# Kernel tuning notes

Measured on AMD Instinct MI355X. Metric: run time of the kernel, lower is better.

## Reference

```python
import jax, jax.numpy as jnp
import numpy as np

N, E = 100000, 3200000
IN, HID, OUT, ED = 16, 64, 32, 3
BN_EPS = 1e-5


def setup_inputs() -> dict:
    key = jax.random.key(0)
    ks = jax.random.split(key, 40)
    d = {}
    d["x"] = jax.random.normal(ks[0], (N, IN), jnp.float32)
    d["edge_index"] = jax.random.randint(ks[1], (2, E), 0, N, dtype=jnp.int32)
    d["edge_attr"] = jax.random.normal(ks[2], (E, ED), jnp.float32)
    i = [3]
    def p(shape):
        w = jax.random.normal(ks[i[0]], shape, jnp.float32) * 0.05
        i[0] += 1
        return w
    for tag, nd in (("inj1", IN), ("inj2", HID), ("inj3", HID)):
        d[tag + "_w1"] = p((ED, nd)); d[tag + "_b1"] = p((nd,))
        d[tag + "_w2"] = p((nd, nd)); d[tag + "_b2"] = p((nd,))
    for tag, ci, co in (("conv1", IN, HID), ("conv2", HID, HID), ("conv3", HID, OUT)):
        d[tag + "_wl"] = p((ci, co)); d[tag + "_bl"] = p((co,))
        d[tag + "_wr"] = p((ci, co))
    for tag, c in (("bn1", HID), ("bn2", HID), ("bn3", OUT)):
        d[tag + "_w"] = p((c,)); d[tag + "_b"] = p((c,))
    return d


def _inject(x, src, dst, edge_attr, w1, b1, w2, b2):
    # edge MLP: [E, ED] -> [E, node_dim], sigmoid wind gate from column 2
    h = jax.nn.relu(edge_attr @ w1 + b1) @ w2 + b2
    gate = jax.nn.sigmoid(edge_attr[:, 2:3])
    msg = h * gate
    agg = jax.ops.segment_sum(msg, dst, num_segments=x.shape[0])
    return x + agg


def _sage(x, src, dst, wl, bl, wr):
    # PyG SAGEConv (mean aggr): lin_l(mean_{j in N(i)} x_j) + lin_r(x_i)
    n = x.shape[0]
    s = jax.ops.segment_sum(x[src], dst, num_segments=n)
    cnt = jax.ops.segment_sum(jnp.ones((src.shape[0], 1), x.dtype), dst, num_segments=n)
    mean = s / jnp.maximum(cnt, 1.0)
    return mean @ wl + bl + x @ wr


def _bn(x, w, b):
    # eval-mode BatchNorm with running_mean=0, running_var=1
    return x * (w / jnp.sqrt(1.0 + BN_EPS)) + b


def reference(x, edge_index, edge_attr,
              inj1_w1, inj1_b1, inj1_w2, inj1_b2,
              inj2_w1, inj2_b1, inj2_w2, inj2_b2,
              inj3_w1, inj3_b1, inj3_w2, inj3_b2,
              conv1_wl, conv1_bl, conv1_wr,
              conv2_wl, conv2_bl, conv2_wr,
              conv3_wl, conv3_bl, conv3_wr,
              bn1_w, bn1_b, bn2_w, bn2_b, bn3_w, bn3_b):
    src, dst = edge_index[0], edge_index[1]
    h = _inject(x, src, dst, edge_attr, inj1_w1, inj1_b1, inj1_w2, inj1_b2)
    h = jax.nn.relu(_bn(_sage(h, src, dst, conv1_wl, conv1_bl, conv1_wr), bn1_w, bn1_b))
    h = _inject(h, src, dst, edge_attr, inj2_w1, inj2_b1, inj2_w2, inj2_b2)
    h = jax.nn.relu(_bn(_sage(h, src, dst, conv2_wl, conv2_bl, conv2_wr), bn2_w, bn2_b))
    h = _inject(h, src, dst, edge_attr, inj3_w1, inj3_b1, inj3_w2, inj3_b2)
    h = jax.nn.relu(_bn(_sage(h, src, dst, conv3_wl, conv3_bl, conv3_wr), bn3_w, bn3_b))
    return h
```

## Files before the change

kernel.cpp:

```cpp
#include <hip/hip_runtime.h>
#include <math.h>

#define N_NODES 100000
#define N_EDGES 3200000
#define NB 391
#define CHUNK 3072
#define NCHUNK 1042
#define HCHUNK 4096
#define NHCHUNK 782
#define CAPB 10240

constexpr size_t al512(size_t x){ return (x + 511) & ~size_t(511); }
constexpr size_t o_bcnt = 0;
constexpr size_t o_bst  = al512(o_bcnt + 512*4);
constexpr size_t o_gb   = al512(o_bst  + 512*4);
constexpr size_t o_off  = al512(o_gb   + 512*4);
constexpr size_t o_srcp = al512(o_off  + ((size_t)N_NODES+1)*4);
constexpr size_t o_epk  = al512(o_srcp + (size_t)N_EDGES*4);
constexpr size_t o_U1   = al512(o_epk  + (size_t)N_EDGES*16);
constexpr size_t o_U2   = al512(o_U1   + (size_t)N_NODES*16*4);
constexpr size_t o_U3   = o_U2 + (size_t)N_NODES*64*4;
constexpr size_t o_gs   = al512(o_U3   + (size_t)N_NODES*64*4);
constexpr size_t o_h1   = al512(o_gs   + (size_t)N_NODES*4);
constexpr size_t o_m1   = al512(o_h1   + (size_t)N_NODES*16*4);
constexpr size_t o_rec  = o_U2;
constexpr size_t o_h2bf = o_epk;
constexpr size_t o_h3bf = o_epk + (size_t)N_NODES*128;
constexpr size_t o_m2   = o_U2;
constexpr size_t o_m3   = o_U2;

#define BN_RSQRT 0.9999950000374997f

__device__ __forceinline__ float4 ld4(const float* p){ return *(const float4*)p; }
__device__ __forceinline__ float fc(const float4& v, int i){ return ((const float*)&v)[i]; }
__device__ __forceinline__ float uf(unsigned u){ return __uint_as_float(u); }

__device__ __forceinline__ unsigned f2bf(float x){
    unsigned u = __float_as_uint(x);
    u += 0x7fffu + ((u >> 16) & 1u);
    return u >> 16;
}

__global__ __launch_bounds__(256) void khistBin(const int* __restrict__ dst,
                                                int* __restrict__ binCnt){
    __shared__ int c[NB];
    int t = threadIdx.x;
    for(int i=t; i<NB; i+=256) c[i] = 0;
    __syncthreads();
    long base = (long)blockIdx.x*HCHUNK;
    int nrem = (int)(N_EDGES - base); if(nrem > HCHUNK) nrem = HCHUNK;
    for(int k=t; k<nrem; k+=256)
        atomicAdd(&c[dst[base+k] >> 8], 1);
    __syncthreads();
    for(int i=t; i<NB; i+=256)
        if(c[i]) atomicAdd(&binCnt[i], c[i]);
}

__global__ __launch_bounds__(512) void kscanBin(const int* __restrict__ binCnt,
                                                int* __restrict__ binStart,
                                                int* __restrict__ gbase){
    __shared__ int s[512];
    int t = threadIdx.x;
    int v = (t < NB) ? binCnt[t] : 0;
    s[t] = v; __syncthreads();
    for(int off=1; off<512; off<<=1){
        int a = (t>=off) ? s[t-off] : 0;
        __syncthreads(); s[t] += a; __syncthreads();
    }
    int ex = (t==0) ? 0 : s[t-1];
    if(t < NB){ binStart[t] = ex; gbase[t] = ex; }
    if(t == NB) binStart[NB] = s[NB-1];
}

__global__ __launch_bounds__(256) void kbinA(const int* __restrict__ src,
                                             const int* __restrict__ dst,
                                             const float* __restrict__ ea,
                                             int* __restrict__ gbase,
                                             unsigned* __restrict__ recD){
    __shared__ int cnt[NB], lofs[NB], gst[NB], lcnt[NB];
    __shared__ int sscan[256];
    __shared__ unsigned stage[CHUNK*4];
    __shared__ unsigned short binOf[CHUNK];
    int t = threadIdx.x;
    long e0i = (long)blockIdx.x*CHUNK;
    int nrem = (int)(N_EDGES - e0i); if(nrem > CHUNK) nrem = CHUNK;
    if(nrem <= 0) return;

    for(int b=t; b<NB; b+=256){ cnt[b]=0; lcnt[b]=0; }
    __syncthreads();
    for(int k=t; k<nrem; k+=256)
        atomicAdd(&cnt[dst[e0i+k] >> 8], 1);
    __syncthreads();
    int c0 = (2*t   < NB) ? cnt[2*t]   : 0;
    int c1 = (2*t+1 < NB) ? cnt[2*t+1] : 0;
    sscan[t] = c0 + c1;
    __syncthreads();
    for(int off=1; off<256; off<<=1){
        int v = (t>=off) ? sscan[t-off] : 0;
        __syncthreads(); sscan[t] += v; __syncthreads();
    }
    int base = (t==0) ? 0 : sscan[t-1];
    if(2*t   < NB) lofs[2*t]   = base;
    if(2*t+1 < NB) lofs[2*t+1] = base + c0;
    for(int b=t; b<NB; b+=256){
        int c = cnt[b];
        gst[b] = c ? atomicAdd(&gbase[b], c) : 0;
    }
    __syncthreads();
    for(int k=t; k<nrem; k+=256){
        long i = e0i + k;
        int d = dst[i];
        int s = src[i];
        float a0 = ea[i*3+0], a1 = ea[i*3+1], a2 = ea[i*3+2];
        int b = d >> 8;
        int p = lofs[b] + atomicAdd(&lcnt[b], 1);
        stage[4*p+0] = (unsigned)s | ((unsigned)(d & 255) << 17);
        stage[4*p+1] = __float_as_uint(a0);
        stage[4*p+2] = __float_as_uint(a1);
        stage[4*p+3] = __float_as_uint(a2);
        binOf[p] = (unsigned short)b;
    }
    __syncthreads();
    int total4 = nrem*4;
    for(int q=t; q<total4; q+=256){
        int p = q >> 2;
        int b = binOf[p];
        int g = gst[b] + (p - lofs[b]);
        recD[(size_t)4*g + (q & 3)] = stage[q];
    }
}

__global__ __launch_bounds__(512) void kbinB(const uint4* __restrict__ rec4,
                                             const int* __restrict__ binStart,
                                             int* __restrict__ offs,
                                             int* __restrict__ srcp,
                                             float4* __restrict__ epk){
    __shared__ int pfx[257], lcnt[256];
    __shared__ int sscan[256];
    __shared__ unsigned short perm[CAPB];
    __shared__ unsigned char  nibOf[CAPB];
    int t = threadIdx.x;
    int b = blockIdx.x;
    int n0 = b*256;
    int nn = N_NODES - n0; if(nn > 256) nn = 256;
    int base = binStart[b];
    int m    = binStart[b+1] - base;
    for(int i=t; i<256; i+=512) lcnt[i] = 0;
    __syncthreads();
    for(int p=t; p<m; p+=512){
        unsigned w0 = ((const unsigned*)rec4)[(size_t)4*(base+p)];
        int nib = (int)((w0 >> 17) & 255u);
        if(p < CAPB) nibOf[p] = (unsigned char)nib;
        atomicAdd(&lcnt[nib], 1);
    }
    __syncthreads();
    if(t < 256) sscan[t] = lcnt[t];
    __syncthreads();
    if(t < 256){
        for(int off=1; off<256; off<<=1){
            int v = (t>=off) ? sscan[t-off] : 0;
            __syncthreads(); sscan[t] += v; __syncthreads();
        }
        pfx[t+1] = sscan[t];
        if(t==0) pfx[0] = 0;
    } else {
        for(int off=1; off<256; off<<=1){ __syncthreads(); __syncthreads(); }
    }
    __syncthreads();
    for(int i=t; i<=nn; i+=512) offs[n0+i] = base + pfx[i];
    for(int i=t; i<256; i+=512) lcnt[i] = 0;
    __syncthreads();
    for(int p=t; p<m; p+=512){
        int nib = nibOf[p];
        int slot = pfx[nib] + atomicAdd(&lcnt[nib], 1);
        perm[slot] = (unsigned short)p;
    }
    __syncthreads();
    for(int s=t; s<m; s+=512){
        uint4 r = rec4[(size_t)(base + (int)perm[s])];
        float e2 = uf(r.w);
        float gate = __builtin_amdgcn_rcpf(1.f + __expf(-e2));
        srcp[base+s] = (int)(r.x & 0x1FFFFu);
        epk [base+s] = make_float4(uf(r.y), uf(r.z), e2, gate);
    }
}

struct InjW { float wa1,wb1,wc1,bb1, wa2,wb2,wc2,bb2, wa3,wb3,wc3,bb3; };

__device__ __forceinline__ void edge_acc(const float4& r, const InjW& W,
                                         float& a1, float& a2, float& a3, float& g){
    float h1 = fmaf(r.z,W.wc1, fmaf(r.y,W.wb1, fmaf(r.x,W.wa1, W.bb1)));
    float h2 = fmaf(r.z,W.wc2, fmaf(r.y,W.wb2, fmaf(r.x,W.wa2, W.bb2)));
    float h3 = fmaf(r.z,W.wc3, fmaf(r.y,W.wb3, fmaf(r.x,W.wa3, W.bb3)));
    a1 = fmaf(fmaxf(h1,0.f), r.w, a1);
    a2 = fmaf(fmaxf(h2,0.f), r.w, a2);
    a3 = fmaf(fmaxf(h3,0.f), r.w, a3);
    g += r.w;
}

__global__ void kinject(const float4* __restrict__ epk, const int* __restrict__ offs,
                        const float* __restrict__ w11, const float* __restrict__ b11,
                        const float* __restrict__ w12, const float* __restrict__ b12,
                        const float* __restrict__ w13, const float* __restrict__ b13,
                        float* __restrict__ U1, float* __restrict__ U2,
                        float* __restrict__ U3, float* __restrict__ gsum){
    int gid = blockIdx.x*blockDim.x + threadIdx.x;
    int node = gid >> 6;
    if(node >= N_NODES) return;
    int lane = threadIdx.x & 63;
    int l16  = lane & 15;
    InjW W;
    W.wa1=w11[l16];  W.wb1=w11[16+l16];  W.wc1=w11[32+l16];  W.bb1=b11[l16];
    W.wa2=w12[lane]; W.wb2=w12[64+lane]; W.wc2=w12[128+lane]; W.bb2=b12[lane];
    W.wa3=w13[lane]; W.wb3=w13[64+lane]; W.wc3=w13[128+lane]; W.bb3=b13[lane];
    int beg = offs[node], end = offs[node+1];
    float a1=0.f, a2=0.f, a3=0.f, g=0.f;
    int e = beg;
    for(; e+2<=end; e+=2){
        float4 r0 = epk[e];
        float4 r1 = epk[e+1];
        edge_acc(r0, W, a1, a2, a3, g);
        edge_acc(r1, W, a1, a2, a3, g);
    }
    if(e < end) edge_acc(epk[e], W, a1, a2, a3, g);
    U2[(size_t)node*64 + lane] = a2;
    U3[(size_t)node*64 + lane] = a3;
    if(lane < 16) U1[node*16 + l16] = a1;
    if(lane == 0) gsum[node] = g;
}

__global__ void kgather16(const float* __restrict__ h, const int* __restrict__ srcp,
                          const int* __restrict__ offs, float* __restrict__ m){
    int gid = blockIdx.x*blockDim.x + threadIdx.x;
    int node = gid >> 6;
    if(node >= N_NODES) return;
    int lane = threadIdx.x & 63;
    int q = lane >> 4, d = lane & 15;
    int beg = offs[node], end = offs[node+1];
    float acc = 0.f;
    for(int e=beg+q; e<end; e+=4) acc += h[(size_t)srcp[e]*16 + d];
    acc += __shfl_down(acc, 32);
    acc += __shfl_down(acc, 16);
    if(lane < 16){
        float c = fmaxf((float)(end-beg), 1.f);
        m[node*16 + lane] = acc / c;
    }
}

__global__ void kgather64bf(const unsigned* __restrict__ hbf, const int* __restrict__ srcp,
                            const int* __restrict__ offs, float* __restrict__ m){
    int gid = blockIdx.x*blockDim.x + threadIdx.x;
    int node = gid >> 6;
    if(node >= N_NODES) return;
    int lane = threadIdx.x & 63;
    int half = lane >> 5, c = lane & 31;
    int beg = offs[node], end = offs[node+1];
    float acc0 = 0.f, acc1 = 0.f;
    int e = beg;
    for(; e+4<=end; e+=4){
        int s0 = srcp[e+half], s1 = srcp[e+2+half];
        unsigned w0 = hbf[(size_t)s0*32 + c];
        unsigned w1 = hbf[(size_t)s1*32 + c];
        acc0 += uf(w0<<16); acc1 += uf(w0 & 0xffff0000u);
        acc0 += uf(w1<<16); acc1 += uf(w1 & 0xffff0000u);
    }
    for(; e+2<=end; e+=2){
        int s = srcp[e+half];
        unsigned w = hbf[(size_t)s*32 + c];
        acc0 += uf(w<<16); acc1 += uf(w & 0xffff0000u);
    }
    if(e < end && half == 0){
        int s = srcp[e];
        unsigned w = hbf[(size_t)s*32 + c];
        acc0 += uf(w<<16); acc1 += uf(w & 0xffff0000u);
    }
    acc0 += __shfl_down(acc0, 32);
    acc1 += __shfl_down(acc1, 32);
    if(lane < 32){
        float inv = 1.f / fmaxf((float)(end-beg), 1.f);
        float2 o; o.x = acc0*inv; o.y = acc1*inv;
        *(float2*)(m + (size_t)node*64 + 2*c) = o;
    }
}


__global__ __launch_bounds__(256) void kdense0(const float* __restrict__ x, const float* __restrict__ U1,
                        const float* __restrict__ gs, const float* __restrict__ w2,
                        const float* __restrict__ b2, float* __restrict__ h1){
    __shared__ float sw[256];
    int t = threadIdx.x;
    sw[t] = w2[t];
    __syncthreads();
    int idx = blockIdx.x*256 + t;
    int n = idx >> 4, j = idx & 15;
    float acc = x[idx] + gs[n]*b2[j];
    const float4* row = (const float4*)(U1 + n*16);
    #pragma unroll
    for(int i4=0;i4<4;i4++){
        float4 r = row[i4];
        acc += r.x*sw[(i4*4+0)*16 + j];
        acc += r.y*sw[(i4*4+1)*16 + j];
        acc += r.z*sw[(i4*4+2)*16 + j];
        acc += r.w*sw[(i4*4+3)*16 + j];
    }
    h1[idx] = acc;
}

__global__ __launch_bounds__(256) void kdense1(const float* __restrict__ m1, const float* __restrict__ h1,
                        const float* __restrict__ U2, const float* __restrict__ gs,
                        const float* __restrict__ wl, const float* __restrict__ bl,
                        const float* __restrict__ wr,
                        const float* __restrict__ w2, const float* __restrict__ b2,
                        const float* __restrict__ bnw, const float* __restrict__ bnb,
                        unsigned* __restrict__ h2bf){
    __shared__ float4 swl[16*16];
    __shared__ float4 swr[16*16];
    __shared__ float4 sw2[64*16];
    int t = threadIdx.x;
    swl[t] = ((const float4*)wl)[t];
    swr[t] = ((const float4*)wr)[t];
    #pragma unroll
    for(int k=0;k<4;k++) sw2[t + 256*k] = ((const float4*)w2)[t + 256*k];
    __syncthreads();

    int w = t>>6, l = t&63;
    int jg = l&15, j0 = jg*4, ng = l>>4;
    int nb = blockIdx.x*64 + w*16 + ng*4;
    int nn[4];
    #pragma unroll
    for(int k=0;k<4;k++) nn[k] = (nb+k < N_NODES) ? nb+k : N_NODES-1;

    float a[4][4], b[4][4];
    float4 blv = ld4(bl + j0);
    float4 b2v = ld4(b2 + j0);
    #pragma unroll
    for(int k=0;k<4;k++){
        float g = gs[nn[k]];
        a[k][0]=blv.x; a[k][1]=blv.y; a[k][2]=blv.z; a[k][3]=blv.w;
        b[k][0]=g*b2v.x; b[k][1]=g*b2v.y; b[k][2]=g*b2v.z; b[k][3]=g*b2v.w;
    }
    #pragma unroll
    for(int i=0;i<16;i+=4){
        float4 rm[4], rh[4];
        #pragma unroll
        for(int k=0;k<4;k++){ rm[k] = ld4(m1 + nn[k]*16 + i); rh[k] = ld4(h1 + nn[k]*16 + i); }
        #pragma unroll
        for(int ii=0;ii<4;ii++){
            float4 wL = swl[(i+ii)*16 + jg];
            float4 wR = swr[(i+ii)*16 + jg];
            #pragma unroll
            for(int k=0;k<4;k++){
                float vm = fc(rm[k],ii), vh = fc(rh[k],ii);
                a[k][0] = fmaf(vm,wL.x, fmaf(vh,wR.x, a[k][0]));
                a[k][1] = fmaf(vm,wL.y, fmaf(vh,wR.y, a[k][1]));
                a[k][2] = fmaf(vm,wL.z, fmaf(vh,wR.z, a[k][2]));
                a[k][3] = fmaf(vm,wL.w, fmaf(vh,wR.w, a[k][3]));
            }
        }
    }
    #pragma unroll 4
    for(int i=0;i<64;i+=4){
        float4 ru[4];
        #pragma unroll
        for(int k=0;k<4;k++) ru[k] = ld4(U2 + (size_t)nn[k]*64 + i);
        #pragma unroll
        for(int ii=0;ii<4;ii++){
            float4 wv = sw2[(i+ii)*16 + jg];
            #pragma unroll
            for(int k=0;k<4;k++){
                float vu = fc(ru[k],ii);
                b[k][0] = fmaf(vu,wv.x,b[k][0]);
                b[k][1] = fmaf(vu,wv.y,b[k][1]);
                b[k][2] = fmaf(vu,wv.z,b[k][2]);
                b[k][3] = fmaf(vu,wv.w,b[k][3]);
            }
        }
    }
    float4 bw = ld4(bnw + j0), bb = ld4(bnb + j0);
    #pragma unroll
    for(int k=0;k<4;k++){
        if(nb+k < N_NODES){
            float ox = fmaxf(a[k][0]*(bw.x*BN_RSQRT)+bb.x,0.f) + b[k][0];
            float oy = fmaxf(a[k][1]*(bw.y*BN_RSQRT)+bb.y,0.f) + b[k][1];
            float oz = fmaxf(a[k][2]*(bw.z*BN_RSQRT)+bb.z,0.f) + b[k][2];
            float ow = fmaxf(a[k][3]*(bw.w*BN_RSQRT)+bb.w,0.f) + b[k][3];
            uint2 pk; pk.x = f2bf(ox) | (f2bf(oy)<<16); pk.y = f2bf(oz) | (f2bf(ow)<<16);
            *(uint2*)(h2bf + (size_t)(nb+k)*32 + (j0>>1)) = pk;
        }
    }
}

__global__ __launch_bounds__(256) void kdense2(const float* __restrict__ m2, const unsigned* __restrict__ h2bf,
                        const float* __restrict__ U3, const float* __restrict__ gs,
                        const float* __restrict__ wl, const float* __restrict__ bl,
                        const float* __restrict__ wr,
                        const float* __restrict__ w2, const float* __restrict__ b2,
                        const float* __restrict__ bnw, const float* __restrict__ bnb,
                        unsigned* __restrict__ h3bf){
    __shared__ float4 swl[64*16];
    __shared__ float4 swr[64*16];
    __shared__ float4 sw2[64*16];
    int t = threadIdx.x;
    #pragma unroll
    for(int k=0;k<4;k++){
        swl[t + 256*k] = ((const float4*)wl)[t + 256*k];
        swr[t + 256*k] = ((const float4*)wr)[t + 256*k];
        sw2[t + 256*k] = ((const float4*)w2)[t + 256*k];
    }
    __syncthreads();

    int w = t>>6, l = t&63;
    int jg = l&15, j0 = jg*4, ng = l>>4;
    int nb = blockIdx.x*64 + w*16 + ng*4;
    int nn[4];
    #pragma unroll
    for(int k=0;k<4;k++) nn[k] = (nb+k < N_NODES) ? nb+k : N_NODES-1;

    float a[4][4], b[4][4];
    float4 blv = ld4(bl + j0);
    float4 b2v = ld4(b2 + j0);
    #pragma unroll
    for(int k=0;k<4;k++){
        float g = gs[nn[k]];
        a[k][0]=blv.x; a[k][1]=blv.y; a[k][2]=blv.z; a[k][3]=blv.w;
        b[k][0]=g*b2v.x; b[k][1]=g*b2v.y; b[k][2]=g*b2v.z; b[k][3]=g*b2v.w;
    }
    #pragma unroll 4
    for(int i=0;i<64;i+=4){
        float4 rm[4], rh[4];
        #pragma unroll
        for(int k=0;k<4;k++){
            rm[k] = ld4(m2 + (size_t)nn[k]*64 + i);
            uint2 hw = *(const uint2*)(h2bf + (size_t)nn[k]*32 + (i>>1));
            rh[k].x = uf(hw.x<<16); rh[k].y = uf(hw.x & 0xffff0000u);
            rh[k].z = uf(hw.y<<16); rh[k].w = uf(hw.y & 0xffff0000u);
        }
        #pragma unroll
        for(int ii=0;ii<4;ii++){
            float4 wL = swl[(i+ii)*16 + jg];
            float4 wR = swr[(i+ii)*16 + jg];
            #pragma unroll
            for(int k=0;k<4;k++){
                float vm = fc(rm[k],ii), vh = fc(rh[k],ii);
                a[k][0] = fmaf(vm,wL.x, fmaf(vh,wR.x, a[k][0]));
                a[k][1] = fmaf(vm,wL.y, fmaf(vh,wR.y, a[k][1]));
                a[k][2] = fmaf(vm,wL.z, fmaf(vh,wR.z, a[k][2]));
                a[k][3] = fmaf(vm,wL.w, fmaf(vh,wR.w, a[k][3]));
            }
        }
    }
    #pragma unroll 4
    for(int i=0;i<64;i+=4){
        float4 ru[4];
        #pragma unroll
        for(int k=0;k<4;k++) ru[k] = ld4(U3 + (size_t)nn[k]*64 + i);
        #pragma unroll
        for(int ii=0;ii<4;ii++){
            float4 wv = sw2[(i+ii)*16 + jg];
            #pragma unroll
            for(int k=0;k<4;k++){
                float vu = fc(ru[k],ii);
                b[k][0] = fmaf(vu,wv.x,b[k][0]);
                b[k][1] = fmaf(vu,wv.y,b[k][1]);
                b[k][2] = fmaf(vu,wv.z,b[k][2]);
                b[k][3] = fmaf(vu,wv.w,b[k][3]);
            }
        }
    }
    float4 bw = ld4(bnw + j0), bb = ld4(bnb + j0);
    #pragma unroll
    for(int k=0;k<4;k++){
        if(nb+k < N_NODES){
            float ox = fmaxf(a[k][0]*(bw.x*BN_RSQRT)+bb.x,0.f) + b[k][0];
            float oy = fmaxf(a[k][1]*(bw.y*BN_RSQRT)+bb.y,0.f) + b[k][1];
            float oz = fmaxf(a[k][2]*(bw.z*BN_RSQRT)+bb.z,0.f) + b[k][2];
            float ow = fmaxf(a[k][3]*(bw.w*BN_RSQRT)+bb.w,0.f) + b[k][3];
            uint2 pk; pk.x = f2bf(ox) | (f2bf(oy)<<16); pk.y = f2bf(oz) | (f2bf(ow)<<16);
            *(uint2*)(h3bf + (size_t)(nb+k)*32 + (j0>>1)) = pk;
        }
    }
}

__global__ __launch_bounds__(256) void kdense3(const float* __restrict__ m3, const unsigned* __restrict__ h3bf,
                        const float* __restrict__ wl, const float* __restrict__ bl,
                        const float* __restrict__ wr,
                        const float* __restrict__ bnw, const float* __restrict__ bnb,
                        float* __restrict__ out){
    __shared__ float4 swl[64*8];
    __shared__ float4 swr[64*8];
    int t = threadIdx.x;
    #pragma unroll
    for(int k=0;k<2;k++){
        swl[t + 256*k] = ((const float4*)wl)[t + 256*k];
        swr[t + 256*k] = ((const float4*)wr)[t + 256*k];
    }
    __syncthreads();

    int w = t>>6, l = t&63;
    int jg = l&7, j0 = jg*4, ng = l>>3;
    int nb = blockIdx.x*128 + w*32 + ng*4;
    int nn[4];
    #pragma unroll
    for(int k=0;k<4;k++) nn[k] = (nb+k < N_NODES) ? nb+k : N_NODES-1;

    float a[4][4];
    float4 blv = ld4(bl + j0);
    #pragma unroll
    for(int k=0;k<4;k++){ a[k][0]=blv.x; a[k][1]=blv.y; a[k][2]=blv.z; a[k][3]=blv.w; }
    #pragma unroll 4
    for(int i=0;i<64;i+=4){
        float4 rm[4], rh[4];
        #pragma unroll
        for(int k=0;k<4;k++){
            rm[k] = ld4(m3 + (size_t)nn[k]*64 + i);
            uint2 hw = *(const uint2*)(h3bf + (size_t)nn[k]*32 + (i>>1));
            rh[k].x = uf(hw.x<<16); rh[k].y = uf(hw.x & 0xffff0000u);
            rh[k].z = uf(hw.y<<16); rh[k].w = uf(hw.y & 0xffff0000u);
        }
        #pragma unroll
        for(int ii=0;ii<4;ii++){
            float4 wL = swl[(i+ii)*8 + jg];
            float4 wR = swr[(i+ii)*8 + jg];
            #pragma unroll
            for(int k=0;k<4;k++){
                float vm = fc(rm[k],ii), vh = fc(rh[k],ii);
                a[k][0] = fmaf(vm,wL.x, fmaf(vh,wR.x, a[k][0]));
                a[k][1] = fmaf(vm,wL.y, fmaf(vh,wR.y, a[k][1]));
                a[k][2] = fmaf(vm,wL.z, fmaf(vh,wR.z, a[k][2]));
                a[k][3] = fmaf(vm,wL.w, fmaf(vh,wR.w, a[k][3]));
            }
        }
    }
    float4 bw = ld4(bnw + j0), bb = ld4(bnb + j0);
    #pragma unroll
    for(int k=0;k<4;k++){
        if(nb+k < N_NODES){
            float4 o;
            o.x = fmaxf(a[k][0]*(bw.x*BN_RSQRT)+bb.x,0.f);
            o.y = fmaxf(a[k][1]*(bw.y*BN_RSQRT)+bb.y,0.f);
            o.z = fmaxf(a[k][2]*(bw.z*BN_RSQRT)+bb.z,0.f);
            o.w = fmaxf(a[k][3]*(bw.w*BN_RSQRT)+bb.w,0.f);
            *(float4*)(out + (size_t)(nb+k)*32 + j0) = o;
        }
    }
}

extern "C" void kernel_launch(void* const* d_in, const int* in_sizes, int n_in,
                              void* d_out, int out_size, void* d_ws, size_t ws_size,
                              hipStream_t stream){
    const float* x    = (const float*)d_in[0];
    const int*   ei   = (const int*)  d_in[1];
    const float* ea   = (const float*)d_in[2];
    const float* i1w1 = (const float*)d_in[3];
    const float* i1b1 = (const float*)d_in[4];
    const float* i1w2 = (const float*)d_in[5];
    const float* i1b2 = (const float*)d_in[6];
    const float* i2w1 = (const float*)d_in[7];
    const float* i2b1 = (const float*)d_in[8];
    const float* i2w2 = (const float*)d_in[9];
    const float* i2b2 = (const float*)d_in[10];
    const float* i3w1 = (const float*)d_in[11];
    const float* i3b1 = (const float*)d_in[12];
    const float* i3w2 = (const float*)d_in[13];
    const float* i3b2 = (const float*)d_in[14];
    const float* c1wl = (const float*)d_in[15];
    const float* c1bl = (const float*)d_in[16];
    const float* c1wr = (const float*)d_in[17];
    const float* c2wl = (const float*)d_in[18];
    const float* c2bl = (const float*)d_in[19];
    const float* c2wr = (const float*)d_in[20];
    const float* c3wl = (const float*)d_in[21];
    const float* c3bl = (const float*)d_in[22];
    const float* c3wr = (const float*)d_in[23];
    const float* bn1w = (const float*)d_in[24];
    const float* bn1b = (const float*)d_in[25];
    const float* bn2w = (const float*)d_in[26];
    const float* bn2b = (const float*)d_in[27];
    const float* bn3w = (const float*)d_in[28];
    const float* bn3b = (const float*)d_in[29];

    char* ws = (char*)d_ws;
    int*      bcnt = (int*)     (ws + o_bcnt);
    int*      bst  = (int*)     (ws + o_bst);
    int*      gb   = (int*)     (ws + o_gb);
    int*      offs = (int*)     (ws + o_off);
    int*      srcp = (int*)     (ws + o_srcp);
    float4*   epk  = (float4*)  (ws + o_epk);
    unsigned* recD = (unsigned*)(ws + o_rec);
    float*    U1   = (float*)   (ws + o_U1);
    float*    U2   = (float*)   (ws + o_U2);
    float*    U3   = (float*)   (ws + o_U3);
    float*    gs   = (float*)   (ws + o_gs);
    float*    h1   = (float*)   (ws + o_h1);
    float*    m1   = (float*)   (ws + o_m1);
    unsigned* h2bf = (unsigned*)(ws + o_h2bf);
    unsigned* h3bf = (unsigned*)(ws + o_h3bf);
    float*    m2   = (float*)   (ws + o_m2);
    float*    m3   = (float*)   (ws + o_m3);

    const int* src = ei;
    const int* dst = ei + N_EDGES;

    hipMemsetAsync(bcnt, 0, 512*4, stream);
    khistBin <<<NHCHUNK, 256, 0, stream>>>(dst, bcnt);
    kscanBin <<<1,       512, 0, stream>>>(bcnt, bst, gb);
    kbinA  <<<NCHUNK, 256, 0, stream>>>(src, dst, ea, gb, recD);
    kbinB  <<<NB,     512, 0, stream>>>((const uint4*)recD, bst, offs, srcp, epk);

    kinject <<<N_NODES/4, 256, 0, stream>>>(epk, offs,
                                            i1w1, i1b1, i2w1, i2b1, i3w1, i3b1,
                                            U1, U2, U3, gs);
    kdense0 <<<N_NODES*16/256, 256, 0, stream>>>(x, U1, gs, i1w2, i1b2, h1);
    kgather16<<<N_NODES/4, 256, 0, stream>>>(h1, srcp, offs, m1);
    kdense1 <<<(N_NODES+63)/64, 256, 0, stream>>>(m1, h1, U2, gs,
                                                 c1wl, c1bl, c1wr, i2w2, i2b2,
                                                 bn1w, bn1b, h2bf);
    kgather64bf<<<N_NODES/4, 256, 0, stream>>>(h2bf, srcp, offs, m2);
    kdense2 <<<(N_NODES+63)/64, 256, 0, stream>>>(m2, h2bf, U3, gs,
                                                 c2wl, c2bl, c2wr, i3w2, i3b2,
                                                 bn2w, bn2b, h3bf);
    kgather64bf<<<N_NODES/4, 256, 0, stream>>>(h3bf, srcp, offs, m3);
    kdense3 <<<(N_NODES+127)/128, 256, 0, stream>>>(m3, h3bf, c3wl, c3bl, c3wr,
                                                 bn3w, bn3b, (float*)d_out);
}
```

Baseline: 781.1 us.

## Project before gathering in layer 3, compress bin records, restructure inject and gather lanes

Layer 3 now applies the lin_l weight to each node first (64 to 32 wide, stored as bf16) and then mean-gathers the 32-wide projection, which halves the bytes gathered per edge. The binning records shrink from 4 to 3 words by packing edge attributes 0 and 1 as bf16, and the binning chunk size grows. kinject and kgather64bf are restructured so that 4 edges are processed in parallel per wavefront, followed by shuffle reductions. Rounding the projected features and the edge attributes to bf16 adds precision loss, and there is one extra kernel launch.

```diff
diff --git a/kernel.cpp b/kernel.cpp
--- a/kernel.cpp
+++ b/kernel.cpp
@@ -4,8 +4,8 @@
 #define N_NODES 100000
 #define N_EDGES 3200000
 #define NB 391
-#define CHUNK 3072
-#define NCHUNK 1042
+#define CHUNK 4096
+#define NCHUNK 782
 #define HCHUNK 4096
 #define NHCHUNK 782
 #define CAPB 10240
@@ -27,7 +27,8 @@
 constexpr size_t o_h2bf = o_epk;
 constexpr size_t o_h3bf = o_epk + (size_t)N_NODES*128;
 constexpr size_t o_m2   = o_U2;
-constexpr size_t o_m3   = o_U2;
+constexpr size_t o_y3   = o_U3;
+constexpr size_t o_m3p  = o_U2;
 
 #define BN_RSQRT 0.9999950000374997f
 
@@ -79,7 +80,7 @@
                                              unsigned* __restrict__ recD){
     __shared__ int cnt[NB], lofs[NB], gst[NB], lcnt[NB];
     __shared__ int sscan[256];
-    __shared__ unsigned stage[CHUNK*4];
+    __shared__ unsigned stage[CHUNK*3];
     __shared__ unsigned short binOf[CHUNK];
     int t = threadIdx.x;
     long e0i = (long)blockIdx.x*CHUNK;
@@ -114,23 +115,23 @@
         float a0 = ea[i*3+0], a1 = ea[i*3+1], a2 = ea[i*3+2];
         int b = d >> 8;
         int p = lofs[b] + atomicAdd(&lcnt[b], 1);
-        stage[4*p+0] = (unsigned)s | ((unsigned)(d & 255) << 17);
-        stage[4*p+1] = __float_as_uint(a0);
-        stage[4*p+2] = __float_as_uint(a1);
-        stage[4*p+3] = __float_as_uint(a2);
+        stage[3*p+0] = (unsigned)s | ((unsigned)(d & 255) << 17);
+        stage[3*p+1] = (f2bf(a1)<<16) | f2bf(a0);
+        stage[3*p+2] = __float_as_uint(a2);
         binOf[p] = (unsigned short)b;
     }
     __syncthreads();
-    int total4 = nrem*4;
-    for(int q=t; q<total4; q+=256){
-        int p = q >> 2;
+    int total3 = nrem*3;
+    for(int q=t; q<total3; q+=256){
+        int p = q/3;
+        int r = q - 3*p;
         int b = binOf[p];
         int g = gst[b] + (p - lofs[b]);
-        recD[(size_t)4*g + (q & 3)] = stage[q];
-    }
-}
-
-__global__ __launch_bounds__(512) void kbinB(const uint4* __restrict__ rec4,
+        recD[(size_t)3*g + r] = stage[q];
+    }
+}
+
+__global__ __launch_bounds__(512) void kbinB(const unsigned* __restrict__ recD,
                                              const int* __restrict__ binStart,
                                              int* __restrict__ offs,
                                              int* __restrict__ srcp,
@@ -148,7 +149,7 @@
     for(int i=t; i<256; i+=512) lcnt[i] = 0;
     __syncthreads();
     for(int p=t; p<m; p+=512){
-        unsigned w0 = ((const unsigned*)rec4)[(size_t)4*(base+p)];
+        unsigned w0 = recD[(size_t)3*(base+p)];
         int nib = (int)((w0 >> 17) & 255u);
         if(p < CAPB) nibOf[p] = (unsigned char)nib;
         atomicAdd(&lcnt[nib], 1);
@@ -177,28 +178,16 @@
     }
     __syncthreads();
     for(int s=t; s<m; s+=512){
-        uint4 r = rec4[(size_t)(base + (int)perm[s])];
-        float e2 = uf(r.w);
+        size_t q = (size_t)3*(base + (int)perm[s]);
+        unsigned w0 = recD[q], w1 = recD[q+1], w2 = recD[q+2];
+        float e2 = uf(w2);
         float gate = __builtin_amdgcn_rcpf(1.f + __expf(-e2));
-        srcp[base+s] = (int)(r.x & 0x1FFFFu);
-        epk [base+s] = make_float4(uf(r.y), uf(r.z), e2, gate);
-    }
-}
-
-struct InjW { float wa1,wb1,wc1,bb1, wa2,wb2,wc2,bb2, wa3,wb3,wc3,bb3; };
-
-__device__ __forceinline__ void edge_acc(const float4& r, const InjW& W,
-                                         float& a1, float& a2, float& a3, float& g){
-    float h1 = fmaf(r.z,W.wc1, fmaf(r.y,W.wb1, fmaf(r.x,W.wa1, W.bb1)));
-    float h2 = fmaf(r.z,W.wc2, fmaf(r.y,W.wb2, fmaf(r.x,W.wa2, W.bb2)));
-    float h3 = fmaf(r.z,W.wc3, fmaf(r.y,W.wb3, fmaf(r.x,W.wa3, W.bb3)));
-    a1 = fmaf(fmaxf(h1,0.f), r.w, a1);
-    a2 = fmaf(fmaxf(h2,0.f), r.w, a2);
-    a3 = fmaf(fmaxf(h3,0.f), r.w, a3);
-    g += r.w;
-}
-
-__global__ void kinject(const float4* __restrict__ epk, const int* __restrict__ offs,
+        srcp[base+s] = (int)(w0 & 0x1FFFFu);
+        epk [base+s] = make_float4(uf(w1<<16), uf(w1 & 0xffff0000u), e2, gate);
+    }
+}
+
+__global__ __launch_bounds__(256) void kinject(const float4* __restrict__ epk, const int* __restrict__ offs,
                         const float* __restrict__ w11, const float* __restrict__ b11,
                         const float* __restrict__ w12, const float* __restrict__ b12,
                         const float* __restrict__ w13, const float* __restrict__ b13,
@@ -208,24 +197,62 @@
     int node = gid >> 6;
     if(node >= N_NODES) return;
     int lane = threadIdx.x & 63;
-    int l16  = lane & 15;
-    InjW W;
-    W.wa1=w11[l16];  W.wb1=w11[16+l16];  W.wc1=w11[32+l16];  W.bb1=b11[l16];
-    W.wa2=w12[lane]; W.wb2=w12[64+lane]; W.wc2=w12[128+lane]; W.bb2=b12[lane];
-    W.wa3=w13[lane]; W.wb3=w13[64+lane]; W.wc3=w13[128+lane]; W.bb3=b13[lane];
+    int q = lane >> 4, j = lane & 15;
+    float wa1=w11[j], wb1=w11[16+j], wc1=w11[32+j], bb1=b11[j];
+    float wa2[4], wb2[4], wc2[4], bv2[4], wa3[4], wb3[4], wc3[4], bv3[4];
+    #pragma unroll
+    for(int k=0;k<4;k++){
+        int c = j + 16*k;
+        wa2[k]=w12[c]; wb2[k]=w12[64+c]; wc2[k]=w12[128+c]; bv2[k]=b12[c];
+        wa3[k]=w13[c]; wb3[k]=w13[64+c]; wc3[k]=w13[128+c]; bv3[k]=b13[c];
+    }
     int beg = offs[node], end = offs[node+1];
-    float a1=0.f, a2=0.f, a3=0.f, g=0.f;
-    int e = beg;
-    for(; e+2<=end; e+=2){
-        float4 r0 = epk[e];
-        float4 r1 = epk[e+1];
-        edge_acc(r0, W, a1, a2, a3, g);
-        edge_acc(r1, W, a1, a2, a3, g);
-    }
-    if(e < end) edge_acc(epk[e], W, a1, a2, a3, g);
-    U2[(size_t)node*64 + lane] = a2;
-    U3[(size_t)node*64 + lane] = a3;
-    if(lane < 16) U1[node*16 + l16] = a1;
+    float a1=0.f, g=0.f;
+    float a2[4] = {0.f,0.f,0.f,0.f};
+    float a3[4] = {0.f,0.f,0.f,0.f};
+    for(int e=beg; e<end; e+=8){
+        int ee0 = e + q, ee1 = e + 4 + q;
+        float4 r0 = make_float4(0.f,0.f,0.f,0.f);
+        float4 r1 = make_float4(0.f,0.f,0.f,0.f);
+        if(ee0 < end) r0 = epk[ee0];
+        if(ee1 < end) r1 = epk[ee1];
+        {
+            float h = fmaf(r0.z,wc1, fmaf(r0.y,wb1, fmaf(r0.x,wa1, bb1)));
+            a1 = fmaf(fmaxf(h,0.f), r0.w, a1);
+            #pragma unroll
+            for(int k=0;k<4;k++){
+                float h2 = fmaf(r0.z,wc2[k], fmaf(r0.y,wb2[k], fmaf(r0.x,wa2[k], bv2[k])));
+                a2[k] = fmaf(fmaxf(h2,0.f), r0.w, a2[k]);
+                float h3 = fmaf(r0.z,wc3[k], fmaf(r0.y,wb3[k], fmaf(r0.x,wa3[k], bv3[k])));
+                a3[k] = fmaf(fmaxf(h3,0.f), r0.w, a3[k]);
+            }
+            g += r0.w;
+        }
+        {
+            float h = fmaf(r1.z,wc1, fmaf(r1.y,wb1, fmaf(r1.x,wa1, bb1)));
+            a1 = fmaf(fmaxf(h,0.f), r1.w, a1);
+            #pragma unroll
+            for(int k=0;k<4;k++){
+                float h2 = fmaf(r1.z,wc2[k], fmaf(r1.y,wb2[k], fmaf(r1.x,wa2[k], bv2[k])));
+                a2[k] = fmaf(fmaxf(h2,0.f), r1.w, a2[k]);
+                float h3 = fmaf(r1.z,wc3[k], fmaf(r1.y,wb3[k], fmaf(r1.x,wa3[k], bv3[k])));
+                a3[k] = fmaf(fmaxf(h3,0.f), r1.w, a3[k]);
+            }
+            g += r1.w;
+        }
+    }
+    #pragma unroll
+    for(int k=0;k<4;k++){
+        a2[k] += __shfl_xor(a2[k], 16); a2[k] += __shfl_xor(a2[k], 32);
+        a3[k] += __shfl_xor(a3[k], 16); a3[k] += __shfl_xor(a3[k], 32);
+    }
+    a1 += __shfl_xor(a1, 16); a1 += __shfl_xor(a1, 32);
+    g  += __shfl_xor(g, 16);  g  += __shfl_xor(g, 32);
+    float v2 = (q==0) ? a2[0] : (q==1) ? a2[1] : (q==2) ? a2[2] : a2[3];
+    float v3 = (q==0) ? a3[0] : (q==1) ? a3[1] : (q==2) ? a3[2] : a3[3];
+    U2[(size_t)node*64 + lane] = v2;
+    U3[(size_t)node*64 + lane] = v3;
+    if(lane < 16) U1[node*16 + j] = a1;
     if(lane == 0) gsum[node] = g;
 }
 
@@ -253,33 +280,55 @@
     int node = gid >> 6;
     if(node >= N_NODES) return;
     int lane = threadIdx.x & 63;
-    int half = lane >> 5, c = lane & 31;
+    int q = lane >> 4, j = lane & 15;
     int beg = offs[node], end = offs[node+1];
-    float acc0 = 0.f, acc1 = 0.f;
-    int e = beg;
-    for(; e+4<=end; e+=4){
-        int s0 = srcp[e+half], s1 = srcp[e+2+half];
-        unsigned w0 = hbf[(size_t)s0*32 + c];
-        unsigned w1 = hbf[(size_t)s1*32 + c];
-        acc0 += uf(w0<<16); acc1 += uf(w0 & 0xffff0000u);
-        acc0 += uf(w1<<16); acc1 += uf(w1 & 0xffff0000u);
-    }
-    for(; e+2<=end; e+=2){
-        int s = srcp[e+half];
-        unsigned w = hbf[(size_t)s*32 + c];
-        acc0 += uf(w<<16); acc1 += uf(w & 0xffff0000u);
-    }
-    if(e < end && half == 0){
-        int s = srcp[e];
-        unsigned w = hbf[(size_t)s*32 + c];
-        acc0 += uf(w<<16); acc1 += uf(w & 0xffff0000u);
-    }
-    acc0 += __shfl_down(acc0, 32);
-    acc1 += __shfl_down(acc1, 32);
-    if(lane < 32){
+    float4 acc = make_float4(0.f,0.f,0.f,0.f);
+    for(int e=beg; e<end; e+=4){
+        int ee = e + q;
+        if(ee < end){
+            int s = srcp[ee];
+            uint2 w = *(const uint2*)(hbf + (size_t)s*32 + 2*j);
+            acc.x += uf(w.x<<16); acc.y += uf(w.x & 0xffff0000u);
+            acc.z += uf(w.y<<16); acc.w += uf(w.y & 0xffff0000u);
+        }
+    }
+    acc.x += __shfl_xor(acc.x,16); acc.x += __shfl_xor(acc.x,32);
+    acc.y += __shfl_xor(acc.y,16); acc.y += __shfl_xor(acc.y,32);
+    acc.z += __shfl_xor(acc.z,16); acc.z += __shfl_xor(acc.z,32);
+    acc.w += __shfl_xor(acc.w,16); acc.w += __shfl_xor(acc.w,32);
+    if(lane < 16){
         float inv = 1.f / fmaxf((float)(end-beg), 1.f);
-        float2 o; o.x = acc0*inv; o.y = acc1*inv;
-        *(float2*)(m + (size_t)node*64 + 2*c) = o;
+        float4 o; o.x=acc.x*inv; o.y=acc.y*inv; o.z=acc.z*inv; o.w=acc.w*inv;
+        *(float4*)(m + (size_t)node*64 + 4*j) = o;
+    }
+}
+
+__global__ void kgather32bf(const unsigned* __restrict__ y3, const int* __restrict__ srcp,
+                            const int* __restrict__ offs, float* __restrict__ m){
+    int gid = blockIdx.x*blockDim.x + threadIdx.x;
+    int node = gid >> 6;
+    if(node >= N_NODES) return;
+    int lane = threadIdx.x & 63;
+    int q = lane >> 4, j = lane & 15;
+    int beg = offs[node], end = offs[node+1];
+    float ax=0.f, ay=0.f;
+    for(int e=beg; e<end; e+=8){
+        int ee0 = e + q, ee1 = e + 4 + q;
+        if(ee0 < end){
+            unsigned w = y3[(size_t)srcp[ee0]*16 + j];
+            ax += uf(w<<16); ay += uf(w & 0xffff0000u);
+        }
+        if(ee1 < end){
+            unsigned w = y3[(size_t)srcp[ee1]*16 + j];
+            ax += uf(w<<16); ay += uf(w & 0xffff0000u);
+        }
+    }
+    ax += __shfl_xor(ax,16); ax += __shfl_xor(ax,32);
+    ay += __shfl_xor(ay,16); ay += __shfl_xor(ay,32);
+    if(lane < 16){
+        float inv = 1.f / fmaxf((float)(end-beg), 1.f);
+        float2 o; o.x = ax*inv; o.y = ay*inv;
+        *(float2*)(m + (size_t)node*32 + 2*j) = o;
     }
 }
 
@@ -481,19 +530,13 @@
     }
 }
 
-__global__ __launch_bounds__(256) void kdense3(const float* __restrict__ m3, const unsigned* __restrict__ h3bf,
-                        const float* __restrict__ wl, const float* __restrict__ bl,
-                        const float* __restrict__ wr,
-                        const float* __restrict__ bnw, const float* __restrict__ bnb,
-                        float* __restrict__ out){
+__global__ __launch_bounds__(256) void kproj3(const unsigned* __restrict__ h3bf,
+                                              const float* __restrict__ wl,
+                                              unsigned* __restrict__ y3){
     __shared__ float4 swl[64*8];
-    __shared__ float4 swr[64*8];
-    int t = threadIdx.x;
-    #pragma unroll
-    for(int k=0;k<2;k++){
-        swl[t + 256*k] = ((const float4*)wl)[t + 256*k];
-        swr[t + 256*k] = ((const float4*)wr)[t + 256*k];
-    }
+    int t = threadIdx.x;
+    #pragma unroll
+    for(int k=0;k<2;k++) swl[t + 256*k] = ((const float4*)wl)[t + 256*k];
     __syncthreads();
 
     int w = t>>6, l = t&63;
@@ -504,15 +547,13 @@
     for(int k=0;k<4;k++) nn[k] = (nb+k < N_NODES) ? nb+k : N_NODES-1;
 
     float a[4][4];
-    float4 blv = ld4(bl + j0);
-    #pragma unroll
-    for(int k=0;k<4;k++){ a[k][0]=blv.x; a[k][1]=blv.y; a[k][2]=blv.z; a[k][3]=blv.w; }
+    #pragma unroll
+    for(int k=0;k<4;k++){ a[k][0]=0.f; a[k][1]=0.f; a[k][2]=0.f; a[k][3]=0.f; }
     #pragma unroll 4
     for(int i=0;i<64;i+=4){
-        float4 rm[4], rh[4];
+        float4 rh[4];
         #pragma unroll
         for(int k=0;k<4;k++){
-            rm[k] = ld4(m3 + (size_t)nn[k]*64 + i);
             uint2 hw = *(const uint2*)(h3bf + (size_t)nn[k]*32 + (i>>1));
             rh[k].x = uf(hw.x<<16); rh[k].y = uf(hw.x & 0xffff0000u);
             rh[k].z = uf(hw.y<<16); rh[k].w = uf(hw.y & 0xffff0000u);
@@ -520,14 +561,71 @@
         #pragma unroll
         for(int ii=0;ii<4;ii++){
             float4 wL = swl[(i+ii)*8 + jg];
+            #pragma unroll
+            for(int k=0;k<4;k++){
+                float vh = fc(rh[k],ii);
+                a[k][0] = fmaf(vh,wL.x,a[k][0]);
+                a[k][1] = fmaf(vh,wL.y,a[k][1]);
+                a[k][2] = fmaf(vh,wL.z,a[k][2]);
+                a[k][3] = fmaf(vh,wL.w,a[k][3]);
+            }
+        }
+    }
+    #pragma unroll
+    for(int k=0;k<4;k++){
+        if(nb+k < N_NODES){
+            uint2 pk;
+            pk.x = f2bf(a[k][0]) | (f2bf(a[k][1])<<16);
+            pk.y = f2bf(a[k][2]) | (f2bf(a[k][3])<<16);
+            *(uint2*)(y3 + (size_t)(nb+k)*16 + (j0>>1)) = pk;
+        }
+    }
+}
+
+__global__ __launch_bounds__(256) void kdense3(const float* __restrict__ m3p, const unsigned* __restrict__ h3bf,
+                        const float* __restrict__ bl,
+                        const float* __restrict__ wr,
+                        const float* __restrict__ bnw, const float* __restrict__ bnb,
+                        float* __restrict__ out){
+    __shared__ float4 swr[64*8];
+    int t = threadIdx.x;
+    #pragma unroll
+    for(int k=0;k<2;k++) swr[t + 256*k] = ((const float4*)wr)[t + 256*k];
+    __syncthreads();
+
+    int w = t>>6, l = t&63;
+    int jg = l&7, j0 = jg*4, ng = l>>3;
+    int nb = blockIdx.x*128 + w*32 + ng*4;
+    int nn[4];
+    #pragma unroll
+    for(int k=0;k<4;k++) nn[k] = (nb+k < N_NODES) ? nb+k : N_NODES-1;
+
+    float a[4][4];
+    float4 blv = ld4(bl + j0);
+    #pragma unroll
+    for(int k=0;k<4;k++){
+        float4 mp = ld4(m3p + (size_t)nn[k]*32 + j0);
+        a[k][0]=blv.x+mp.x; a[k][1]=blv.y+mp.y; a[k][2]=blv.z+mp.z; a[k][3]=blv.w+mp.w;
+    }
+    #pragma unroll 4
+    for(int i=0;i<64;i+=4){
+        float4 rh[4];
+        #pragma unroll
+        for(int k=0;k<4;k++){
+            uint2 hw = *(const uint2*)(h3bf + (size_t)nn[k]*32 + (i>>1));
+            rh[k].x = uf(hw.x<<16); rh[k].y = uf(hw.x & 0xffff0000u);
+            rh[k].z = uf(hw.y<<16); rh[k].w = uf(hw.y & 0xffff0000u);
+        }
+        #pragma unroll
+        for(int ii=0;ii<4;ii++){
             float4 wR = swr[(i+ii)*8 + jg];
             #pragma unroll
             for(int k=0;k<4;k++){
-                float vm = fc(rm[k],ii), vh = fc(rh[k],ii);
-                a[k][0] = fmaf(vm,wL.x, fmaf(vh,wR.x, a[k][0]));
-                a[k][1] = fmaf(vm,wL.y, fmaf(vh,wR.y, a[k][1]));
-                a[k][2] = fmaf(vm,wL.z, fmaf(vh,wR.z, a[k][2]));
-                a[k][3] = fmaf(vm,wL.w, fmaf(vh,wR.w, a[k][3]));
+                float vh = fc(rh[k],ii);
+                a[k][0] = fmaf(vh,wR.x,a[k][0]);
+                a[k][1] = fmaf(vh,wR.y,a[k][1]);
+                a[k][2] = fmaf(vh,wR.z,a[k][2]);
+                a[k][3] = fmaf(vh,wR.w,a[k][3]);
             }
         }
     }
@@ -596,7 +694,8 @@
     unsigned* h2bf = (unsigned*)(ws + o_h2bf);
     unsigned* h3bf = (unsigned*)(ws + o_h3bf);
     float*    m2   = (float*)   (ws + o_m2);
-    float*    m3   = (float*)   (ws + o_m3);
+    unsigned* y3   = (unsigned*)(ws + o_y3);
+    float*    m3p  = (float*)   (ws + o_m3p);
 
     const int* src = ei;
     const int* dst = ei + N_EDGES;
@@ -605,7 +704,7 @@
     khistBin <<<NHCHUNK, 256, 0, stream>>>(dst, bcnt);
     kscanBin <<<1,       512, 0, stream>>>(bcnt, bst, gb);
     kbinA  <<<NCHUNK, 256, 0, stream>>>(src, dst, ea, gb, recD);
-    kbinB  <<<NB,     512, 0, stream>>>((const uint4*)recD, bst, offs, srcp, epk);
+    kbinB  <<<NB,     512, 0, stream>>>(recD, bst, offs, srcp, epk);
 
     kinject <<<N_NODES/4, 256, 0, stream>>>(epk, offs,
                                             i1w1, i1b1, i2w1, i2b1, i3w1, i3b1,
@@ -619,7 +718,8 @@
     kdense2 <<<(N_NODES+63)/64, 256, 0, stream>>>(m2, h2bf, U3, gs,
                                                  c2wl, c2bl, c2wr, i3w2, i3b2,
                                                  bn2w, bn2b, h3bf);
-    kgather64bf<<<N_NODES/4, 256, 0, stream>>>(h3bf, srcp, offs, m3);
-    kdense3 <<<(N_NODES+127)/128, 256, 0, stream>>>(m3, h3bf, c3wl, c3bl, c3wr,
+    kproj3  <<<(N_NODES+127)/128, 256, 0, stream>>>(h3bf, c3wl, y3);
+    kgather32bf<<<N_NODES/4, 256, 0, stream>>>(y3, srcp, offs, m3p);
+    kdense3 <<<(N_NODES+127)/128, 256, 0, stream>>>(m3p, h3bf, c3bl, c3wr,
                                                  bn3w, bn3b, (float*)d_out);
 }
```

Measured after the change: 750.3 us. 3.9% less time.
